# Kernel tuning notes

Measured on AMD Instinct MI355X. Metric: run time of the kernel, lower is better.

## Reference

```python
import jax, jax.numpy as jnp
import numpy as np

IN_F = 128
OUT_F = 128
SCALE = float(np.sqrt(OUT_F))

def swish(x):
    return x * jax.nn.sigmoid(x)

def setup_inputs() -> dict:
    key = jax.random.key(0)
    ks = jax.random.split(key, 10)
    B, A = 4, 4096
    s = 1.0 / np.sqrt(IN_F)
    return {
        "x": jax.random.normal(ks[0], (B, A, IN_F), dtype=jnp.float32),
        "connectivity": jax.random.normal(ks[1], (B, A, A), dtype=jnp.float32),
        "Wq": jax.random.uniform(ks[2], (IN_F, OUT_F), jnp.float32, -s, s),
        "Wk": jax.random.uniform(ks[3], (IN_F, OUT_F), jnp.float32, -s, s),
        "Wv": jax.random.uniform(ks[4], (IN_F, OUT_F), jnp.float32, -s, s),
        "W1": jax.random.uniform(ks[5], (OUT_F, OUT_F), jnp.float32, -s, s),
        "b1": jnp.zeros((OUT_F,), jnp.float32),
        "W2": jax.random.uniform(ks[6], (OUT_F, OUT_F), jnp.float32, -s, s),
        "b2": jnp.zeros((OUT_F,), jnp.float32),
        "gamma": jnp.ones((OUT_F,), jnp.float32),
        "beta": jnp.zeros((OUT_F,), jnp.float32),
    }

def reference(x, connectivity, Wq, Wk, Wv, W1, b1, W2, b2, gamma, beta):
    # Q,K,V projections (no bias): [B,A,D]
    Q = jnp.einsum('bah,hd->bad', x, Wq)
    K = jnp.einsum('bah,hd->bad', x, Wk)
    V = jnp.einsum('bah,hd->bad', x, Wv)
    # dense all-pairs scores with additive connectivity bias: [B,A,A]
    scores = jnp.einsum('bqd,bkd->bqk', Q, K) / SCALE + connectivity
    alpha = jax.nn.softmax(scores, axis=-1)
    # dropout p=0.0 / eval mode -> identity
    H = jnp.einsum('bqk,bkd->bqd', alpha, V)
    # Swish-MLP tail
    h = swish(H)
    h = h @ W1 + b1
    h = swish(h)
    h = h @ W2 + b2
    # LayerNorm over last dim (eps=1e-5 as torch default)
    mu = jnp.mean(h, axis=-1, keepdims=True)
    var = jnp.var(h, axis=-1, keepdims=True)
    return (h - mu) * jax.lax.rsqrt(var + 1e-5) * gamma + beta
```

## Files before the change

kernel.cpp:

```cpp
#include <hip/hip_runtime.h>

#define L2E 1.44269504088896340736f
#define INV_SCALE 0.08838834764831845f

typedef _Float16 half8 __attribute__((ext_vector_type(8)));
typedef _Float16 half4 __attribute__((ext_vector_type(4)));
typedef float f32x4 __attribute__((ext_vector_type(4)));

__device__ __forceinline__ float exp2_fast(float x) {
#if __has_builtin(__builtin_amdgcn_exp2f)
  return __builtin_amdgcn_exp2f(x);
#else
  return exp2f(x);
#endif
}

__device__ __forceinline__ f32x4 mfma16(half8 a, half8 b, f32x4 c) {
  return __builtin_amdgcn_mfma_f32_16x16x32_f16(a, b, c, 0, 0, 0);
}

__device__ __forceinline__ void gload16(const void* g, void* l) {
  __builtin_amdgcn_global_load_lds(
      (const __attribute__((address_space(1))) void*)g,
      (__attribute__((address_space(3))) void*)l, 16, 0, 0);
}

__device__ __forceinline__ float swish_f(float v) {
  return v / (1.f + exp2_fast(-L2E * v));
}

template <int CTRL>
__device__ __forceinline__ float dppmov(float x) {
  int xi = __builtin_bit_cast(int, x);
  int r = __builtin_amdgcn_update_dpp(xi, xi, CTRL, 0xf, 0xf, false);
  return __builtin_bit_cast(float, r);
}
__device__ __forceinline__ float red16_sum(float x) {
  x += dppmov<0xB1>(x);
  x += dppmov<0x4E>(x);
  x += dppmov<0x141>(x);
  x += dppmov<0x140>(x);
  return x;
}

__global__ __launch_bounds__(256) void prep_kernel(
    const float* __restrict__ Wq, const float* __restrict__ Wk,
    const float* __restrict__ Wv, const float* __restrict__ W1,
    const float* __restrict__ W2, _Float16* __restrict__ Wf) {
  const int g = blockIdx.x * 256 + threadIdx.x;
  const int mat = g >> 11, rem = g & 2047;
  const int f = rem >> 6, lane = rem & 63;
  const int n = (f >> 2) * 16 + (lane & 15);
  const int k0 = (f & 3) * 32 + (lane >> 4) * 8;
  const float* W = (mat == 0) ? Wq : (mat == 1) ? Wk : (mat == 2) ? Wv
                   : (mat == 3) ? W1 : W2;
  half8 h;
#pragma unroll
  for (int j = 0; j < 8; ++j) h[j] = (_Float16)W[(k0 + j) * 128 + n];
  *(half8*)(Wf + (size_t)g * 8) = h;
}

__global__ __launch_bounds__(256) void kv_kernel(
    const float* __restrict__ x, const _Float16* __restrict__ Wf,
    _Float16* __restrict__ Kg, _Float16* __restrict__ Vg) {
  __shared__ __align__(16) _Float16 sc[64 * 136];
  const int tid = threadIdx.x;
  const int w = tid >> 6, lane = tid & 63;
  const int n16 = lane & 15, quad = lane >> 4;
  const int blk = blockIdx.x;

  half8 xf[4];
  {
    const float* xr = x + (size_t)(blk * 64 + w * 16 + n16) * 128 + quad * 8;
#pragma unroll
    for (int kc = 0; kc < 4; ++kc) {
      float4 a = *(const float4*)(xr + kc * 32);
      float4 b = *(const float4*)(xr + kc * 32 + 4);
      half8 h;
      h[0] = (_Float16)a.x; h[1] = (_Float16)a.y;
      h[2] = (_Float16)a.z; h[3] = (_Float16)a.w;
      h[4] = (_Float16)b.x; h[5] = (_Float16)b.y;
      h[6] = (_Float16)b.z; h[7] = (_Float16)b.w;
      xf[kc] = h;
    }
  }

  for (int mat = 0; mat < 2; ++mat) {
    f32x4 acc[8];
#pragma unroll
    for (int ct = 0; ct < 8; ++ct) acc[ct] = f32x4{0.f, 0.f, 0.f, 0.f};
#pragma unroll
    for (int ct = 0; ct < 8; ++ct)
#pragma unroll
      for (int kc = 0; kc < 4; ++kc) {
        half8 wf = *(const half8*)(Wf +
            ((size_t)((mat + 1) * 32 + ct * 4 + kc) * 64 + lane) * 8);
        acc[ct] = mfma16(xf[kc], wf, acc[ct]);
      }
#pragma unroll
    for (int ct = 0; ct < 8; ++ct)
#pragma unroll
      for (int r = 0; r < 4; ++r)
        sc[(w * 16 + quad * 4 + r) * 136 + ct * 16 + n16] = (_Float16)acc[ct][r];
    __syncthreads();

    if (mat == 0) {
#pragma unroll
      for (int i = 0; i < 4; ++i) {
        const int c = tid + 256 * i;
        const int ln = c & 63, kc = (c >> 6) & 3, ct = (c >> 8) & 1, tl = (c >> 9) & 1;
        half8 v = *(const half8*)&sc[(tl * 32 + ct * 16 + (ln & 15)) * 136 +
                                     kc * 32 + (ln >> 4) * 8];
        *(half8*)(Kg + ((((size_t)(blk * 2 + tl)) * 2 + ct) * 4 + kc) * 512 + ln * 8) = v;
      }
    } else {
#pragma unroll
      for (int i = 0; i < 4; ++i) {
        const int c = tid + 256 * i;
        const int ln = c & 63, dt = (c >> 6) & 7, tl = (c >> 9) & 1;
        const int q2 = ln >> 4, nn = ln & 15;
        half8 v;
#pragma unroll
        for (int j = 0; j < 8; ++j)
          v[j] = sc[(tl * 32 + q2 * 8 + j) * 136 + dt * 16 + nn];
        *(half8*)(Vg + (((size_t)(blk * 2 + tl)) * 8 + dt) * 512 + ln * 8) = v;
      }
    }
    __syncthreads();
  }
}

template <int NW>
__global__ __launch_bounds__(NW * 64) void flash_kernel(
    const float* __restrict__ x, const float* __restrict__ conn,
    const _Float16* __restrict__ Wf,
    const _Float16* __restrict__ Kg, const _Float16* __restrict__ Vg,
    _Float16* __restrict__ Og, float2* __restrict__ Ml,
    int nsplit, int nt) {
  __shared__ __align__(16) _Float16 kb[2][4096];
  __shared__ __align__(16) _Float16 vb[2][4096];
  __shared__ __align__(16) _Float16 pb[NW][656];
  __shared__ __align__(16) float alb[NW][16];

  const int tid = threadIdx.x, w = tid >> 6, lane = tid & 63;
  const int n16 = lane & 15, quad = lane >> 4;
  const int bid = blockIdx.x;
  int batch, sk, rg;
  if (nsplit == 4) {
    batch = bid & 3; sk = (bid >> 2) & 3; rg = bid >> 4;
  } else if (nsplit == 2) {
    batch = bid & 3; sk = (bid >> 2) & 1; rg = bid >> 3;
  } else {
    batch = bid & 3; sk = 0; rg = bid >> 2;
  }
  const int rt_g = batch * 256 + rg * NW + w;
  const int t0 = sk * nt;
  const int rowb = rg * (NW * 16) + w * 16 + n16;

  _Float16* scratch = (w < 2) ? &kb[w][0] : &vb[w - 2][0];

  half8 qf[4];
  {
    half8 xf[4];
    const float* xr = x + ((size_t)batch * 4096 + rowb) * 128 + quad * 8;
#pragma unroll
    for (int kc = 0; kc < 4; ++kc) {
      float4 a = *(const float4*)(xr + kc * 32);
      float4 b = *(const float4*)(xr + kc * 32 + 4);
      half8 h;
      h[0] = (_Float16)a.x; h[1] = (_Float16)a.y;
      h[2] = (_Float16)a.z; h[3] = (_Float16)a.w;
      h[4] = (_Float16)b.x; h[5] = (_Float16)b.y;
      h[6] = (_Float16)b.z; h[7] = (_Float16)b.w;
      xf[kc] = h;
    }
    _Float16* tw = scratch;
#pragma unroll
    for (int ct = 0; ct < 8; ++ct) {
      f32x4 aq = f32x4{0.f, 0.f, 0.f, 0.f};
#pragma unroll
      for (int kc = 0; kc < 4; ++kc) {
        half8 wf = *(const half8*)(Wf + ((size_t)(ct * 4 + kc) * 64 + lane) * 8);
        aq = mfma16(xf[kc], wf, aq);
      }
#pragma unroll
      for (int r = 0; r < 4; ++r)
        tw[(quad * 4 + r) * 136 + ct * 16 + n16] = (_Float16)aq[r];
    }
#pragma unroll
    for (int kc = 0; kc < 4; ++kc)
      qf[kc] = *(const half8*)(tw + n16 * 136 + kc * 32 + quad * 8);
  }
  __syncthreads();

  const _Float16* kp = Kg + (size_t)batch * 524288 + (size_t)t0 * 4096 + tid * 8;
  const _Float16* vp = Vg + (size_t)batch * 524288 + (size_t)t0 * 4096 + tid * 8;
  const float* cp = conn + (size_t)batch * 16777216 + (size_t)rowb * 4096 +
                    (size_t)t0 * 32 + quad * 4;
  const int wbase = (tid & ~63) * 8;
  constexpr int NC = 8 / NW;

  auto stage = [&](int t, int buf) {
    const _Float16* ks = kp + (size_t)t * 4096;
    const _Float16* vs = vp + (size_t)t * 4096;
#pragma unroll
    for (int c = 0; c < NC; ++c) {
      gload16(ks + c * (NW * 512), &kb[buf][c * (NW * 512) + wbase]);
      gload16(vs + c * (NW * 512), &vb[buf][c * (NW * 512) + wbase]);
    }
  };
  auto ldconn = [&](int i, float4* cr) {
    const float* c0 = cp + (size_t)i * 32;
    cr[0] = *(const float4*)c0;
    cr[1] = *(const float4*)(c0 + 16);
  };

  f32x4 o[8];
#pragma unroll
  for (int dt = 0; dt < 8; ++dt) o[dt] = f32x4{0.f, 0.f, 0.f, 0.f};
  float m_i = -__builtin_inff();
  float l_i = 0.f;

  float4 ca[2], cb[2];
  stage(0, 0);
  ldconn(0, ca);
  __syncthreads();

  auto compute = [&](int buf, const float4* cc) {
    f32x4 s0 = f32x4{0.f, 0.f, 0.f, 0.f};
    f32x4 s1 = f32x4{0.f, 0.f, 0.f, 0.f};
    const _Float16* kc_ = kb[buf];
#pragma unroll
    for (int kc = 0; kc < 4; ++kc) {
      half8 kf0 = *(const half8*)&kc_[kc * 512 + lane * 8];
      half8 kf1 = *(const half8*)&kc_[(4 + kc) * 512 + lane * 8];
      s0 = mfma16(kf0, qf[kc], s0);
      s1 = mfma16(kf1, qf[kc], s1);
    }
    float pr[8];
#pragma unroll
    for (int r = 0; r < 4; ++r) {
      pr[r] = fmaf(s0[r], INV_SCALE, cc[0][r]);
      pr[4 + r] = fmaf(s1[r], INV_SCALE, cc[1][r]);
    }
    float mx = pr[0];
#pragma unroll
    for (int c = 1; c < 8; ++c) mx = fmaxf(mx, pr[c]);
    mx = fmaxf(mx, __shfl_xor(mx, 16, 64));
    mx = fmaxf(mx, __shfl_xor(mx, 32, 64));
    if (__any(mx > m_i)) {
      const float mn = fmaxf(m_i, mx);
      const float al = exp2_fast((m_i - mn) * L2E);
      m_i = mn;
      l_i *= al;
      if (quad == 0) alb[w][n16] = al;
      const float4 av = *(const float4*)&alb[w][quad * 4];
#pragma unroll
      for (int dt = 0; dt < 8; ++dt)
#pragma unroll
        for (int r = 0; r < 4; ++r) o[dt][r] *= av[r];
    }
    const float nm = -m_i * L2E;
#pragma unroll
    for (int c = 0; c < 8; ++c) pr[c] = exp2_fast(fmaf(pr[c], L2E, nm));
    float sm = pr[0];
#pragma unroll
    for (int c = 1; c < 8; ++c) sm += pr[c];
    sm += __shfl_xor(sm, 16, 64);
    sm += __shfl_xor(sm, 32, 64);
    l_i += sm;
    _Float16* pw = pb[w];
    half4 p0, p1;
#pragma unroll
    for (int r = 0; r < 4; ++r) {
      p0[r] = (_Float16)pr[r];
      p1[r] = (_Float16)pr[4 + r];
    }
    *(half4*)(pw + n16 * 40 + quad * 4) = p0;
    *(half4*)(pw + n16 * 40 + 16 + quad * 4) = p1;
    half8 pf = *(const half8*)(pw + n16 * 40 + quad * 8);
    const _Float16* vc = vb[buf];
#pragma unroll
    for (int dt = 0; dt < 8; ++dt) {
      half8 vf = *(const half8*)&vc[dt * 512 + lane * 8];
      o[dt] = mfma16(pf, vf, o[dt]);
    }
  };

#pragma unroll 1
  for (int i = 0; i < nt; i += 2) {
    stage(i + 1, 1);
    ldconn(i + 1, cb);
    compute(0, ca);
    __syncthreads();
    if (i + 2 < nt) {
      stage(i + 2, 0);
      ldconn(i + 2, ca);
    }
    compute(1, cb);
    __syncthreads();
  }

  if (quad == 0) alb[w][n16] = l_i;
  const float4 lv = *(const float4*)&alb[w][quad * 4];
  float il[4];
#pragma unroll
  for (int r = 0; r < 4; ++r) il[r] = 1.f / lv[r];
  _Float16* tw = scratch;
#pragma unroll
  for (int dt = 0; dt < 8; ++dt)
#pragma unroll
    for (int r = 0; r < 4; ++r)
      tw[(quad * 4 + r) * 136 + dt * 16 + n16] = (_Float16)(o[dt][r] * il[r]);
  _Float16* ob = Og + ((size_t)(sk * 1024 + rt_g) * 4) * 512;
#pragma unroll
  for (int kc = 0; kc < 4; ++kc) {
    half8 of = *(const half8*)(tw + n16 * 136 + kc * 32 + quad * 8);
    *(half8*)(ob + kc * 512 + lane * 8) = of;
  }
  if (quad == 0)
    Ml[sk * 16384 + rt_g * 16 + n16] = make_float2(m_i, l_i);
}

__global__ __launch_bounds__(256) void mlp_kernel(
    const _Float16* __restrict__ Og, const float2* __restrict__ Ml,
    const _Float16* __restrict__ Wf,
    const float* __restrict__ b1, const float* __restrict__ b2,
    const float* __restrict__ gamma, const float* __restrict__ beta,
    float* __restrict__ out, int nsplit) {
  __shared__ __align__(16) _Float16 hb[4][2176];
  const int tid = threadIdx.x, w = tid >> 6, lane = tid & 63;
  const int n16 = lane & 15, quad = lane >> 4;
  const int rt_g = blockIdx.x * 4 + w;

  float2 ml[4];
  float m = -__builtin_inff();
  for (int s = 0; s < nsplit; ++s) {
    ml[s] = Ml[s * 16384 + rt_g * 16 + n16];
    m = fmaxf(m, ml[s].x);
  }
  float wgt[4], wsum = 0.f;
  for (int s = 0; s < nsplit; ++s) {
    wgt[s] = ml[s].y * exp2_fast((ml[s].x - m) * L2E);
    wsum += wgt[s];
  }
  const float inv = 1.f / wsum;

  half8 hf[4];
#pragma unroll
  for (int kc = 0; kc < 4; ++kc) {
    float hv[8] = {0, 0, 0, 0, 0, 0, 0, 0};
    for (int s = 0; s < nsplit; ++s) {
      half8 ofr = *(const half8*)(Og +
          ((size_t)(s * 1024 + rt_g) * 4 + kc) * 512 + lane * 8);
#pragma unroll
      for (int j = 0; j < 8; ++j) hv[j] += wgt[s] * (float)ofr[j];
    }
    half8 h;
#pragma unroll
    for (int j = 0; j < 8; ++j) h[j] = (_Float16)swish_f(hv[j] * inv);
    hf[kc] = h;
  }

  float b1v[8], b2v[8], gv[8], bv[8];
#pragma unroll
  for (int ct = 0; ct < 8; ++ct) {
    b1v[ct] = b1[ct * 16 + n16];
    b2v[ct] = b2[ct * 16 + n16];
    gv[ct] = gamma[ct * 16 + n16];
    bv[ct] = beta[ct * 16 + n16];
  }

  f32x4 acc[8];
#pragma unroll
  for (int ct = 0; ct < 8; ++ct) acc[ct] = f32x4{0.f, 0.f, 0.f, 0.f};
#pragma unroll
  for (int ct = 0; ct < 8; ++ct)
#pragma unroll
    for (int kc = 0; kc < 4; ++kc) {
      half8 wf = *(const half8*)(Wf +
          ((size_t)(3 * 32 + ct * 4 + kc) * 64 + lane) * 8);
      acc[ct] = mfma16(hf[kc], wf, acc[ct]);
    }
  _Float16* hw = hb[w];
#pragma unroll
  for (int ct = 0; ct < 8; ++ct)
#pragma unroll
    for (int r = 0; r < 4; ++r)
      hw[(quad * 4 + r) * 136 + ct * 16 + n16] =
          (_Float16)swish_f(acc[ct][r] + b1v[ct]);
  half8 h1f[4];
#pragma unroll
  for (int kc = 0; kc < 4; ++kc)
    h1f[kc] = *(const half8*)(hw + n16 * 136 + kc * 32 + quad * 8);

#pragma unroll
  for (int ct = 0; ct < 8; ++ct) acc[ct] = f32x4{0.f, 0.f, 0.f, 0.f};
#pragma unroll
  for (int ct = 0; ct < 8; ++ct)
#pragma unroll
    for (int kc = 0; kc < 4; ++kc) {
      half8 wf = *(const half8*)(Wf +
          ((size_t)(4 * 32 + ct * 4 + kc) * 64 + lane) * 8);
      acc[ct] = mfma16(h1f[kc], wf, acc[ct]);
    }
  float hx[8][4];
  float sm[4] = {0, 0, 0, 0}, ss[4] = {0, 0, 0, 0};
#pragma unroll
  for (int ct = 0; ct < 8; ++ct)
#pragma unroll
    for (int r = 0; r < 4; ++r) {
      const float v = acc[ct][r] + b2v[ct];
      hx[ct][r] = v;
      sm[r] += v;
      ss[r] += v * v;
    }
#pragma unroll
  for (int r = 0; r < 4; ++r) {
    sm[r] = red16_sum(sm[r]);
    ss[r] = red16_sum(ss[r]);
  }
#pragma unroll
  for (int r = 0; r < 4; ++r) {
    const float mu = sm[r] * (1.f / 128.f);
    const float var = ss[r] * (1.f / 128.f) - mu * mu;
    const float rstd = rsqrtf(var + 1e-5f);
    const size_t row = (size_t)rt_g * 16 + quad * 4 + r;
#pragma unroll
    for (int ct = 0; ct < 8; ++ct)
      out[row * 128 + ct * 16 + n16] = (hx[ct][r] - mu) * rstd * gv[ct] + bv[ct];
  }
}

extern "C" void kernel_launch(void* const* d_in, const int* in_sizes, int n_in,
                              void* d_out, int out_size, void* d_ws,
                              size_t ws_size, hipStream_t stream) {
  const float* x     = (const float*)d_in[0];
  const float* conn  = (const float*)d_in[1];
  const float* Wq    = (const float*)d_in[2];
  const float* Wk    = (const float*)d_in[3];
  const float* Wv    = (const float*)d_in[4];
  const float* W1    = (const float*)d_in[5];
  const float* b1    = (const float*)d_in[6];
  const float* W2    = (const float*)d_in[7];
  const float* b2    = (const float*)d_in[8];
  const float* gamma = (const float*)d_in[9];
  const float* beta  = (const float*)d_in[10];
  float* out = (float*)d_out;

  const size_t baseElems = (size_t)81920 + 2 * 2097152;
  const size_t need4 =
      (baseElems + 4 * 2097152) * 2 + 4 * 16384 * sizeof(float2);
  const size_t need2 =
      (baseElems + 2 * 2097152) * 2 + 2 * 16384 * sizeof(float2);
  const int nsplit = (ws_size >= need4) ? 4 : (ws_size >= need2) ? 2 : 1;
  const int nt = 128 / nsplit;

  _Float16* Wf = (_Float16*)d_ws;
  _Float16* Kg = Wf + 81920;
  _Float16* Vg = Kg + 2097152;
  _Float16* Og = Vg + 2097152;
  float2* Ml = (float2*)(Og + (size_t)2097152 * nsplit);

  prep_kernel<<<40, 256, 0, stream>>>(Wq, Wk, Wv, W1, W2, Wf);
  kv_kernel<<<256, 256, 0, stream>>>(x, Wf, Kg, Vg);
  if (nsplit == 4) {
    flash_kernel<4><<<1024, 256, 0, stream>>>(x, conn, Wf, Kg, Vg, Og, Ml,
                                              nsplit, nt);
  } else if (nsplit == 2) {
    flash_kernel<2><<<1024, 128, 0, stream>>>(x, conn, Wf, Kg, Vg, Og, Ml,
                                              nsplit, nt);
  } else {
    flash_kernel<2><<<512, 128, 0, stream>>>(x, conn, Wf, Kg, Vg, Og, Ml,
                                             nsplit, nt);
  }
  mlp_kernel<<<256, 256, 0, stream>>>(Og, Ml, Wf, b1, b2, gamma, beta, out,
                                      nsplit);
}
```

Baseline: 475.0 us.

## Deepen K/V/conn prefetch with counted vmcnt waits and raise MFMA priority

Restructures the flash-attention main loop so that two tiles are in flight before the loop starts. Each stage now waits only with a partial s_waitcnt vmcnt instead of draining all loads through __syncthreads, and raw s_barrier plus sched_barrier keep the compiler from reordering. It also wraps the QK and PV MFMA blocks in s_setprio(1) so matrix work is favored when waves contend. The aim is more overlap of global-to-LDS loads and the connectivity reads with compute. The risk is that the hand-counted vmcnt (PP) becomes wrong if the number of load instructions per stage changes.

```diff
diff --git a/kernel.cpp b/kernel.cpp
--- a/kernel.cpp
+++ b/kernel.cpp
@@ -199,6 +199,7 @@
                     (size_t)t0 * 32 + quad * 4;
   const int wbase = (tid & ~63) * 8;
   constexpr int NC = 8 / NW;
+  constexpr int PP = 2 * NC + 2;
 
   auto stage = [&](int t, int buf) {
     const _Float16* ks = kp + (size_t)t * 4096;
@@ -221,15 +222,11 @@
   float m_i = -__builtin_inff();
   float l_i = 0.f;
 
-  float4 ca[2], cb[2];
-  stage(0, 0);
-  ldconn(0, ca);
-  __syncthreads();
-
   auto compute = [&](int buf, const float4* cc) {
     f32x4 s0 = f32x4{0.f, 0.f, 0.f, 0.f};
     f32x4 s1 = f32x4{0.f, 0.f, 0.f, 0.f};
     const _Float16* kc_ = kb[buf];
+    __builtin_amdgcn_s_setprio(1);
 #pragma unroll
     for (int kc = 0; kc < 4; ++kc) {
       half8 kf0 = *(const half8*)&kc_[kc * 512 + lane * 8];
@@ -237,6 +234,7 @@
       s0 = mfma16(kf0, qf[kc], s0);
       s1 = mfma16(kf1, qf[kc], s1);
     }
+    __builtin_amdgcn_s_setprio(0);
     float pr[8];
 #pragma unroll
     for (int r = 0; r < 4; ++r) {
@@ -280,26 +278,52 @@
     *(half4*)(pw + n16 * 40 + 16 + quad * 4) = p1;
     half8 pf = *(const half8*)(pw + n16 * 40 + quad * 8);
     const _Float16* vc = vb[buf];
+    __builtin_amdgcn_s_setprio(1);
 #pragma unroll
     for (int dt = 0; dt < 8; ++dt) {
       half8 vf = *(const half8*)&vc[dt * 512 + lane * 8];
       o[dt] = mfma16(pf, vf, o[dt]);
     }
+    __builtin_amdgcn_s_setprio(0);
   };
 
+  float4 ca[2], cb[2];
+  stage(0, 0);
+  ldconn(0, ca);
+  stage(1, 1);
+  ldconn(1, cb);
+
 #pragma unroll 1
-  for (int i = 0; i < nt; i += 2) {
-    stage(i + 1, 1);
-    ldconn(i + 1, cb);
+  for (int t = 0; t < nt; t += 2) {
+    asm volatile("s_waitcnt vmcnt(%0)" ::"n"(PP));
+    __builtin_amdgcn_sched_barrier(0);
+    __builtin_amdgcn_s_barrier();
+    __builtin_amdgcn_sched_barrier(0);
     compute(0, ca);
-    __syncthreads();
-    if (i + 2 < nt) {
-      stage(i + 2, 0);
-      ldconn(i + 2, ca);
-    }
+    if (t + 2 < nt) {
+      __builtin_amdgcn_sched_barrier(0);
+      __builtin_amdgcn_s_barrier();
+      stage(t + 2, 0);
+      ldconn(t + 2, ca);
+    }
+    if (t + 2 < nt) {
+      asm volatile("s_waitcnt vmcnt(%0)" ::"n"(PP));
+    } else {
+      asm volatile("s_waitcnt vmcnt(0)");
+    }
+    __builtin_amdgcn_sched_barrier(0);
+    __builtin_amdgcn_s_barrier();
+    __builtin_amdgcn_sched_barrier(0);
     compute(1, cb);
-    __syncthreads();
-  }
+    if (t + 3 < nt) {
+      __builtin_amdgcn_sched_barrier(0);
+      __builtin_amdgcn_s_barrier();
+      stage(t + 3, 1);
+      ldconn(t + 3, cb);
+    }
+  }
+  __builtin_amdgcn_sched_barrier(0);
+  __builtin_amdgcn_s_barrier();
 
   if (quad == 0) alb[w][n16] = l_i;
   const float4 lv = *(const float4*)&alb[w][quad * 4];
```

After: 477.3 us. Within noise of the previous version (+0.5%).
